# Kernel optimization log

Measured on AMD Instinct MI355X. Metric: run time of the kernel, lower is better.

The kernel has to match this reference:

```python
import jax, jax.numpy as jnp
import numpy as np

B, M, R = 1024, 2048, 8192  # batch of states, metabolites, reactions
SPARSITY = 0.002            # ~4 nonzero substrates / products per reaction


def setup_inputs() -> dict:
    key = jax.random.key(0)
    k1, k2, k3, k4, k5, k6 = jax.random.split(key, 6)
    # concentrations must be strictly positive (log used in power-law eval)
    conc = jax.random.uniform(k1, (B, M), minval=1e-3, maxval=1.0, dtype=jnp.float32)
    # sparse kinetic-order (exponent) matrix: ~4 substrates/reaction, order 1 or 2
    e_mask = jax.random.bernoulli(k2, SPARSITY, (M, R))
    E = jnp.where(e_mask, jax.random.randint(k3, (M, R), 1, 3), 0).astype(jnp.int32)
    # sparse stoichiometry matrix with coefficients in {-2,-1,1,2}
    s_mask = jax.random.bernoulli(k4, SPARSITY, (M, R))
    s_raw = jax.random.randint(k5, (M, R), 0, 4)
    s_val = jnp.where(s_raw < 2, s_raw - 2, s_raw - 1)  # {-2,-1,1,2}
    S = jnp.where(s_mask, s_val, 0).astype(jnp.int32)
    # per-reaction rate constants (the learned ParameterDict)
    k = jax.random.uniform(k6, (R,), minval=0.1, maxval=2.0, dtype=jnp.float32)
    return {"conc": conc, "E": E, "S": S, "k": k}


def reference(conc, E, S, k):
    # mass-action rate laws: v_j = k_j * prod_i c_i^{E_ij}, evaluated in log-space
    # logc: [B, M]; Ef: [M, R] -> v: [B, R]
    logc = jnp.log(conc)
    Ef = E.astype(conc.dtype)
    v = k * jnp.exp(jnp.einsum('bm,mr->br', logc, Ef))
    # stoichiometric ODE RHS: dX/dt = v @ S^T -> [B, M]
    Sf = S.astype(conc.dtype)
    dXdt = jnp.einsum('br,mr->bm', v, Sf)
    return dXdt
```

## Files before the change

kernel.cpp:

```cpp
#include <hip/hip_runtime.h>
#include <hip/hip_fp16.h>

#define Bsz 1024
#define Mm  2048
#define Rr  8192
#define EMAX 32
#define SMAX 64

typedef unsigned short ushort_t;

__global__ __launch_bounds__(256) void zero_ecnt(int* __restrict__ p) {
    p[blockIdx.x * 256 + threadIdx.x] = 0;
}

__global__ __launch_bounds__(256) void prep_kernel(
    const float* __restrict__ conc, const int* __restrict__ E,
    __half2* __restrict__ logcTh2, int* __restrict__ ecnt, ushort_t* __restrict__ elist)
{
    __shared__ int smem[64 * 65 + 1];
    const int bid = blockIdx.x;
    const int t   = threadIdx.x;

    if (bid < 512) {
        float (*tile)[65] = (float(*)[65])smem;
        const int mt = (bid & 31) * 64;
        const int bt = (bid >> 5) * 64;
        const int lm = t & 63;
        const int w  = t >> 6;
        for (int i = w; i < 64; i += 4)
            tile[lm][i] = __logf(conc[(size_t)(bt + i) * Mm + mt + lm]);
        __syncthreads();
        const int s       = bt >> 7;
        const int colbase = (bt & 127) >> 1;
        __half2* dst = logcTh2 + (size_t)s * (Mm * 64);
        for (int idx = t; idx < 64 * 32; idx += 256) {
            const int j = idx >> 5, bp = idx & 31;
            dst[(mt + j) * 64 + colbase + bp] =
                __floats2half2_rn(tile[j][2 * bp], tile[j][2 * bp + 1]);
        }
    } else {
        const int m = bid - 512;
        int* buf = smem;
        int* nh  = smem + 256;
        if (t == 0) *nh = 0;
        __syncthreads();
        const int4* E4 = (const int4*)E + (size_t)m * 2048;
        int4 ev[8];
        #pragma unroll
        for (int u = 0; u < 8; ++u) ev[u] = E4[t + 256 * u];
        #pragma unroll
        for (int u = 0; u < 8; ++u) {
            const int r0 = (t + 256 * u) << 2;
            int v[4] = {ev[u].x, ev[u].y, ev[u].z, ev[u].w};
            #pragma unroll
            for (int q = 0; q < 4; ++q)
                if (v[q]) {
                    int i = atomicAdd(nh, 1);
                    if (i < 256) buf[i] = (v[q] << 13) | (r0 + q);
                }
        }
        __syncthreads();
        const int en = min(*nh, 256);
        if (t < en) {
            int wv = buf[t];
            int r  = wv & 0x1FFF;
            int e  = wv >> 13;
            int slot = atomicAdd(&ecnt[r], 1);
            if (slot < EMAX) elist[r * EMAX + slot] = (ushort_t)((e << 11) | m);
        }
    }
}

__global__ __launch_bounds__(256) void rs_kernel(
    const __half2* __restrict__ logcTh2, const float* __restrict__ kvec,
    const int* __restrict__ ecnt, const ushort_t* __restrict__ elist,
    const int* __restrict__ S, int* __restrict__ scnt, ushort_t* __restrict__ slist,
    __half2* __restrict__ VTh)
{
    __shared__ int smem[257];
    const int bid   = blockIdx.x;
    const int t     = threadIdx.x;
    const int grp   = bid >> 3;
    const int lane8 = bid & 7;

    if ((grp & 1) == 0) {
        const int m = (grp >> 1) * 8 + lane8;
        int* buf = smem;
        int* nh  = smem + 256;
        if (t == 0) *nh = 0;
        __syncthreads();
        const int4* S4 = (const int4*)S + (size_t)m * 2048;
        int4 sv[8];
        #pragma unroll
        for (int u = 0; u < 8; ++u) sv[u] = S4[t + 256 * u];
        #pragma unroll
        for (int u = 0; u < 8; ++u) {
            const int r0 = (t + 256 * u) << 2;
            int v[4] = {sv[u].x, sv[u].y, sv[u].z, sv[u].w};
            #pragma unroll
            for (int q = 0; q < 4; ++q)
                if (v[q]) {
                    int i = atomicAdd(nh, 1);
                    if (i < 256) buf[i] = ((v[q] + 2) << 13) | (r0 + q);
                }
        }
        __syncthreads();
        const int sn = min(*nh, SMAX);
        if (t == 0) scnt[m] = sn;
        if (t < SMAX)
            slist[m * SMAX + t] = (t < sn) ? (ushort_t)buf[t]
                                           : (ushort_t)0x4000;
        return;
    }
    const int s   = lane8;
    const int rch = grp >> 1;
    const int col = t & 63;
    const int wr  = __builtin_amdgcn_readfirstlane(t >> 6);
    const __half2* lc = logcTh2 + (size_t)s * (Mm * 64);
    __half2* vt = VTh + (size_t)s * (Rr * 64);
    const int rb = rch * 32 + wr * 8;

    int  cnt[8]; int2 L0[8]; float kk[8];
    #pragma unroll
    for (int i = 0; i < 8; ++i) {
        const int r = rb + i;
        cnt[i] = min(ecnt[r], EMAX);
        L0[i]  = *(const int2*)(elist + (r << 5));
        kk[i]  = kvec[r];
    }
    float2 acc[8];
    #pragma unroll
    for (int h = 0; h < 2; ++h) {
        int ad[16]; float wg[16];
        #pragma unroll
        for (int i = 0; i < 4; ++i) {
            const int ii = h * 4 + i;
            const unsigned wx = (unsigned)L0[ii].x, wy = (unsigned)L0[ii].y;
            ad[4 * i + 0] = (int)(wx & 0x7FFu) * 64 + col;
            ad[4 * i + 1] = (int)((wx >> 16) & 0x7FFu) * 64 + col;
            ad[4 * i + 2] = (int)(wy & 0x7FFu) * 64 + col;
            ad[4 * i + 3] = (int)((wy >> 16) & 0x7FFu) * 64 + col;
            wg[4 * i + 0] = (cnt[ii] > 0) ? (float)((wx & 0xFFFFu) >> 11) : 0.f;
            wg[4 * i + 1] = (cnt[ii] > 1) ? (float)(wx >> 27) : 0.f;
            wg[4 * i + 2] = (cnt[ii] > 2) ? (float)((wy & 0xFFFFu) >> 11) : 0.f;
            wg[4 * i + 3] = (cnt[ii] > 3) ? (float)(wy >> 27) : 0.f;
        }
        __half2 gv[16];
        #pragma unroll
        for (int j = 0; j < 16; ++j) gv[j] = lc[ad[j]];
        #pragma unroll
        for (int i = 0; i < 4; ++i) {
            const int ii = h * 4 + i;
            float2 a = make_float2(0.f, 0.f);
            #pragma unroll
            for (int q = 0; q < 4; ++q) {
                const float2 gg = __half22float2(gv[4 * i + q]);
                a.x += wg[4 * i + q] * gg.x;
                a.y += wg[4 * i + q] * gg.y;
            }
            acc[ii] = a;
        }
    }
    {
        unsigned w; float2 g; float v0, v1;
        #define EG2(word, c0, c1, A)                                           \
            w = (unsigned)(word);                                              \
            v0 = (c0) ? (float)((w & 0xFFFF) >> 11) : 0.f;                     \
            v1 = (c1) ? (float)(w >> 27) : 0.f;                                \
            g = __half22float2(lc[(w & 0x7FF) * 64 + col]);                    \
            A.x += v0 * g.x;  A.y += v0 * g.y;                                 \
            g = __half22float2(lc[((w >> 16) & 0x7FF) * 64 + col]);            \
            A.x += v1 * g.x;  A.y += v1 * g.y;
        #pragma unroll
        for (int i = 0; i < 8; ++i) {
            for (int j = 4; j < cnt[i]; j += 4) {
                int2 T = *(const int2*)(elist + ((rb + i) << 5) + j);
                EG2(T.x, j + 0 < cnt[i], j + 1 < cnt[i], acc[i])
                EG2(T.y, j + 2 < cnt[i], j + 3 < cnt[i], acc[i])
            }
        }
        #undef EG2
    }
    #pragma unroll
    for (int i = 0; i < 8; ++i)
        vt[(rb + i) * 64 + col] =
            __floats2half2_rn(kk[i] * __expf(acc[i].x), kk[i] * __expf(acc[i].y));
}

__global__ __launch_bounds__(256) void assemble_kernel(
    const __half2* __restrict__ VTh, const int* __restrict__ scnt,
    const ushort_t* __restrict__ slist, float* __restrict__ out)
{
    __shared__ float tile[128][17];
    const int s   = blockIdx.x & 7;
    const int mch = blockIdx.x >> 3;
    const int col = threadIdx.x & 63;
    const int wm  = __builtin_amdgcn_readfirstlane(threadIdx.x >> 6);
    const __half2* vt = VTh + (size_t)s * (Rr * 64);
    const int m0 = mch * 16;

    int scn[4]; int4 W0[4], W1[4];
    #pragma unroll
    for (int i = 0; i < 4; ++i) {
        const int m = m0 + i * 4 + wm;
        scn[i] = min(scnt[m], SMAX);
        W0[i]  = *(const int4*)(slist + (m << 6));
        W1[i]  = *(const int4*)(slist + (m << 6) + 8);
    }
    #pragma unroll
    for (int i = 0; i < 4; ++i) {
        const int ml = i * 4 + wm;
        const unsigned wd[8] = {(unsigned)W0[i].x, (unsigned)W0[i].y,
                                (unsigned)W0[i].z, (unsigned)W0[i].w,
                                (unsigned)W1[i].x, (unsigned)W1[i].y,
                                (unsigned)W1[i].z, (unsigned)W1[i].w};
        int ad[16]; float swt[16];
        #pragma unroll
        for (int q = 0; q < 8; ++q) {
            const unsigned lo = wd[q] & 0xFFFFu, hi = wd[q] >> 16;
            ad[2 * q + 0]  = (int)(lo & 0x1FFFu) * 64 + col;
            ad[2 * q + 1]  = (int)(hi & 0x1FFFu) * 64 + col;
            swt[2 * q + 0] = (float)((int)(lo >> 13) - 2);
            swt[2 * q + 1] = (float)((int)(hi >> 13) - 2);
        }
        __half2 gv[16];
        #pragma unroll
        for (int q = 0; q < 16; ++q) gv[q] = vt[ad[q]];
        float2 a = make_float2(0.f, 0.f);
        #pragma unroll
        for (int q = 0; q < 16; ++q) {
            const float2 gg = __half22float2(gv[q]);
            a.x += swt[q] * gg.x;
            a.y += swt[q] * gg.y;
        }
        {
            unsigned w; float2 v; float sw;
            #define SG(word, A)                                                \
                w = (unsigned)(word);                                          \
                v = __half22float2(vt[(w & 0x1FFF) * 64 + col]);               \
                sw = (float)((int)((w & 0xFFFF) >> 13) - 2);                   \
                A.x += sw * v.x;  A.y += sw * v.y;                             \
                v = __half22float2(vt[((w >> 16) & 0x1FFF) * 64 + col]);       \
                sw = (float)((int)(w >> 29) - 2);                              \
                A.x += sw * v.x;  A.y += sw * v.y;
            for (int j = 16; j < scn[i]; j += 8) {
                int4 T = *(const int4*)(slist + ((m0 + ml) << 6) + j);
                SG(T.x, a) SG(T.y, a) SG(T.z, a) SG(T.w, a)
            }
            #undef SG
        }
        tile[2 * col][ml]     = a.x;
        tile[2 * col + 1][ml] = a.y;
    }
    __syncthreads();
    #pragma unroll
    for (int pass = 0; pass < 2; ++pass) {
        const int bl = (threadIdx.x >> 2) + pass * 64;
        const int fl = threadIdx.x & 3;
        float4 vv = *(const float4*)&tile[bl][fl * 4];
        *(float4*)(out + (size_t)(s * 128 + bl) * Mm + m0 + fl * 4) = vv;
    }
}

extern "C" void kernel_launch(void* const* d_in, const int* in_sizes, int n_in,
                              void* d_out, int out_size, void* d_ws, size_t ws_size,
                              hipStream_t stream) {
    const float* conc = (const float*)d_in[0];
    const int*   E    = (const int*)d_in[1];
    const int*   S    = (const int*)d_in[2];
    const float* kvec = (const float*)d_in[3];
    float* out = (float*)d_out;

    __half2* VTh     = (__half2*)d_ws;
    __half2* logcTh2 = (__half2*)((char*)d_ws + (size_t)Rr * Bsz * sizeof(__half));
    int*    ecnt     = (int*)((char*)logcTh2 + (size_t)Mm * Bsz * sizeof(__half));
    int*    scnt     = ecnt + Rr;
    ushort_t* elist  = (ushort_t*)(scnt + Mm);
    ushort_t* slist  = elist + Rr * EMAX;
    const size_t need = (size_t)Rr * Bsz * sizeof(__half)
                      + (size_t)Mm * Bsz * sizeof(__half)
                      + (size_t)(Rr + Mm) * sizeof(int)
                      + (size_t)(Rr * EMAX + Mm * SMAX) * sizeof(ushort_t);
    if (ws_size < need) return;

    zero_ecnt<<<32, 256, 0, stream>>>(ecnt);
    prep_kernel<<<2560, 256, 0, stream>>>(conc, E, logcTh2, ecnt, elist);
    rs_kernel<<<4096, 256, 0, stream>>>(logcTh2, kvec, ecnt, elist, S, scnt, slist, VTh);
    assemble_kernel<<<1024, 256, 0, stream>>>(VTh, scnt, slist, out);
}
```

Baseline: 175.5 us.

## Stage sparse gathers through LDS via global_load_lds in rate and assemble kernels

Replaces the register-destined gather loads of logc and rate values with direct global-to-LDS loads (global_load_lds), staged in per-wave LDS buffers. Each wave then waits on vmcnt and reads the staged values back from LDS. Both kernels also get an occupancy hint of 4 blocks per CU. The intent is to issue all 32 or 16 gathers at once with lower register pressure and better latency hiding, at the cost of extra LDS traffic, a full wait barrier, and a larger LDS footprint that may limit occupancy.

```diff
diff --git a/kernel.cpp b/kernel.cpp
--- a/kernel.cpp
+++ b/kernel.cpp
@@ -71,13 +71,13 @@
     }
 }
 
-__global__ __launch_bounds__(256) void rs_kernel(
+__global__ __launch_bounds__(256, 4) void rs_kernel(
     const __half2* __restrict__ logcTh2, const float* __restrict__ kvec,
     const int* __restrict__ ecnt, const ushort_t* __restrict__ elist,
     const int* __restrict__ S, int* __restrict__ scnt, ushort_t* __restrict__ slist,
     __half2* __restrict__ VTh)
 {
-    __shared__ int smem[257];
+    __shared__ int smem[8192];
     const int bid   = blockIdx.x;
     const int t     = threadIdx.x;
     const int grp   = bid >> 3;
@@ -128,38 +128,45 @@
         L0[i]  = *(const int2*)(elist + (r << 5));
         kk[i]  = kvec[r];
     }
+    char* st = (char*)smem + wr * 8192 / 4 * 4;
+    st = (char*)smem + wr * 8192;
+    float wg[32];
+    #pragma unroll
+    for (int i = 0; i < 8; ++i) {
+        const unsigned wx = (unsigned)L0[i].x, wy = (unsigned)L0[i].y;
+        const int m0_ = (int)(wx & 0x7FFu),  m1_ = (int)((wx >> 16) & 0x7FFu);
+        const int m2_ = (int)(wy & 0x7FFu),  m3_ = (int)((wy >> 16) & 0x7FFu);
+        wg[4 * i + 0] = (cnt[i] > 0) ? (float)((wx & 0xFFFFu) >> 11) : 0.f;
+        wg[4 * i + 1] = (cnt[i] > 1) ? (float)(wx >> 27) : 0.f;
+        wg[4 * i + 2] = (cnt[i] > 2) ? (float)((wy & 0xFFFFu) >> 11) : 0.f;
+        wg[4 * i + 3] = (cnt[i] > 3) ? (float)(wy >> 27) : 0.f;
+        __builtin_amdgcn_global_load_lds(
+            (const __attribute__((address_space(1))) void*)(lc + m0_ * 64 + col),
+            (__attribute__((address_space(3))) void*)(st + (4 * i + 0) * 256), 4, 0, 0);
+        __builtin_amdgcn_global_load_lds(
+            (const __attribute__((address_space(1))) void*)(lc + m1_ * 64 + col),
+            (__attribute__((address_space(3))) void*)(st + (4 * i + 1) * 256), 4, 0, 0);
+        __builtin_amdgcn_global_load_lds(
+            (const __attribute__((address_space(1))) void*)(lc + m2_ * 64 + col),
+            (__attribute__((address_space(3))) void*)(st + (4 * i + 2) * 256), 4, 0, 0);
+        __builtin_amdgcn_global_load_lds(
+            (const __attribute__((address_space(1))) void*)(lc + m3_ * 64 + col),
+            (__attribute__((address_space(3))) void*)(st + (4 * i + 3) * 256), 4, 0, 0);
+    }
+    asm volatile("s_waitcnt vmcnt(0)" ::: "memory");
+    __builtin_amdgcn_sched_barrier(0);
     float2 acc[8];
     #pragma unroll
-    for (int h = 0; h < 2; ++h) {
-        int ad[16]; float wg[16];
-        #pragma unroll
-        for (int i = 0; i < 4; ++i) {
-            const int ii = h * 4 + i;
-            const unsigned wx = (unsigned)L0[ii].x, wy = (unsigned)L0[ii].y;
-            ad[4 * i + 0] = (int)(wx & 0x7FFu) * 64 + col;
-            ad[4 * i + 1] = (int)((wx >> 16) & 0x7FFu) * 64 + col;
-            ad[4 * i + 2] = (int)(wy & 0x7FFu) * 64 + col;
-            ad[4 * i + 3] = (int)((wy >> 16) & 0x7FFu) * 64 + col;
-            wg[4 * i + 0] = (cnt[ii] > 0) ? (float)((wx & 0xFFFFu) >> 11) : 0.f;
-            wg[4 * i + 1] = (cnt[ii] > 1) ? (float)(wx >> 27) : 0.f;
-            wg[4 * i + 2] = (cnt[ii] > 2) ? (float)((wy & 0xFFFFu) >> 11) : 0.f;
-            wg[4 * i + 3] = (cnt[ii] > 3) ? (float)(wy >> 27) : 0.f;
-        }
-        __half2 gv[16];
-        #pragma unroll
-        for (int j = 0; j < 16; ++j) gv[j] = lc[ad[j]];
-        #pragma unroll
-        for (int i = 0; i < 4; ++i) {
-            const int ii = h * 4 + i;
-            float2 a = make_float2(0.f, 0.f);
-            #pragma unroll
-            for (int q = 0; q < 4; ++q) {
-                const float2 gg = __half22float2(gv[4 * i + q]);
-                a.x += wg[4 * i + q] * gg.x;
-                a.y += wg[4 * i + q] * gg.y;
-            }
-            acc[ii] = a;
-        }
+    for (int i = 0; i < 8; ++i) {
+        float2 a = make_float2(0.f, 0.f);
+        #pragma unroll
+        for (int q = 0; q < 4; ++q) {
+            const __half2 h = *(const __half2*)(st + (4 * i + q) * 256 + col * 4);
+            const float2 gg = __half22float2(h);
+            a.x += wg[4 * i + q] * gg.x;
+            a.y += wg[4 * i + q] * gg.y;
+        }
+        acc[i] = a;
     }
     {
         unsigned w; float2 g; float v0, v1;
@@ -187,11 +194,12 @@
             __floats2half2_rn(kk[i] * __expf(acc[i].x), kk[i] * __expf(acc[i].y));
 }
 
-__global__ __launch_bounds__(256) void assemble_kernel(
+__global__ __launch_bounds__(256, 4) void assemble_kernel(
     const __half2* __restrict__ VTh, const int* __restrict__ scnt,
     const ushort_t* __restrict__ slist, float* __restrict__ out)
 {
     __shared__ float tile[128][17];
+    __shared__ char  stg[4][4096];
     const int s   = blockIdx.x & 7;
     const int mch = blockIdx.x >> 3;
     const int col = threadIdx.x & 63;
@@ -207,6 +215,7 @@
         W0[i]  = *(const int4*)(slist + (m << 6));
         W1[i]  = *(const int4*)(slist + (m << 6) + 8);
     }
+    char* st = stg[wm];
     #pragma unroll
     for (int i = 0; i < 4; ++i) {
         const int ml = i * 4 + wm;
@@ -214,22 +223,26 @@
                                 (unsigned)W0[i].z, (unsigned)W0[i].w,
                                 (unsigned)W1[i].x, (unsigned)W1[i].y,
                                 (unsigned)W1[i].z, (unsigned)W1[i].w};
-        int ad[16]; float swt[16];
+        float swt[16];
         #pragma unroll
         for (int q = 0; q < 8; ++q) {
             const unsigned lo = wd[q] & 0xFFFFu, hi = wd[q] >> 16;
-            ad[2 * q + 0]  = (int)(lo & 0x1FFFu) * 64 + col;
-            ad[2 * q + 1]  = (int)(hi & 0x1FFFu) * 64 + col;
             swt[2 * q + 0] = (float)((int)(lo >> 13) - 2);
             swt[2 * q + 1] = (float)((int)(hi >> 13) - 2);
-        }
-        __half2 gv[16];
-        #pragma unroll
-        for (int q = 0; q < 16; ++q) gv[q] = vt[ad[q]];
+            __builtin_amdgcn_global_load_lds(
+                (const __attribute__((address_space(1))) void*)(vt + (int)(lo & 0x1FFFu) * 64 + col),
+                (__attribute__((address_space(3))) void*)(st + (2 * q + 0) * 256), 4, 0, 0);
+            __builtin_amdgcn_global_load_lds(
+                (const __attribute__((address_space(1))) void*)(vt + (int)(hi & 0x1FFFu) * 64 + col),
+                (__attribute__((address_space(3))) void*)(st + (2 * q + 1) * 256), 4, 0, 0);
+        }
+        asm volatile("s_waitcnt vmcnt(0)" ::: "memory");
+        __builtin_amdgcn_sched_barrier(0);
         float2 a = make_float2(0.f, 0.f);
         #pragma unroll
         for (int q = 0; q < 16; ++q) {
-            const float2 gg = __half22float2(gv[q]);
+            const __half2 h = *(const __half2*)(st + q * 256 + col * 4);
+            const float2 gg = __half22float2(h);
             a.x += swt[q] * gg.x;
             a.y += swt[q] * gg.y;
         }
```

Result: no change. 179.0 us (+2.0%).
